# Performance work log

Measured on AMD Instinct MI355X. Metric: run time of the kernel, lower is better.

The kernel has to match this reference:

```python
import jax, jax.numpy as jnp
import numpy as np

N, E, G = 200000, 400000, 4096
EMB, FEAT, L = 300, 256, 5
NUM_ATOM, NUM_CHI, NUM_BOND, NUM_DIR = 119, 3, 5, 3


def setup_inputs() -> dict:
    key = jax.random.key(0)
    ks = jax.random.split(key, 24)
    s = 0.1
    return {
        "x": jax.random.randint(ks[0], (N, 2), 0, 3),
        "edge_index": jax.random.randint(ks[1], (2, E), 0, N),
        "edge_attr": jax.random.randint(ks[2], (E, 2), 0, 3),
        "batch": jnp.sort(jax.random.randint(ks[3], (N,), 0, G)),
        # node-type embeddings
        "x_emb1": jax.random.normal(ks[4], (NUM_ATOM, EMB)) * s,
        "x_emb2": jax.random.normal(ks[5], (NUM_CHI, EMB)) * s,
        # per-layer GCN params (stacked over L layers)
        "W": jax.random.normal(ks[6], (L, EMB, EMB)) * s,
        "b": jnp.zeros((L, EMB)),
        "e1": jax.random.normal(ks[7], (L, NUM_BOND, 1)) * s,
        "e2": jax.random.normal(ks[8], (L, NUM_DIR, 1)) * s,
        # batchnorm params
        "gamma": jnp.ones((L, EMB)),
        "beta": jnp.zeros((L, EMB)),
        # heads
        "feat_W": jax.random.normal(ks[9], (EMB, FEAT)) * s,
        "feat_b": jnp.zeros((FEAT,)),
        "out_W1": jax.random.normal(ks[10], (FEAT, FEAT)) * s,
        "out_b1": jnp.zeros((FEAT,)),
        "out_W2": jax.random.normal(ks[11], (FEAT, FEAT // 2)) * s,
        "out_b2": jnp.zeros((FEAT // 2,)),
    }


def reference(x, edge_index, edge_attr, batch, x_emb1, x_emb2, W, b, e1, e2,
              gamma, beta, feat_W, feat_b, out_W1, out_b1, out_W2, out_b2):
    n = x.shape[0]
    loop = jnp.arange(n, dtype=edge_index.dtype)
    # add self loops: edge type 4, direction 0
    src = jnp.concatenate([edge_index[0], loop])
    dst = jnp.concatenate([edge_index[1], loop])
    ea0 = jnp.concatenate([edge_attr[:, 0], jnp.full((n,), 4, edge_attr.dtype)])
    ea1 = jnp.concatenate([edge_attr[:, 1], jnp.zeros((n,), edge_attr.dtype)])

    h = x_emb1[x[:, 0]] + x_emb2[x[:, 1]]  # [N, EMB]
    for l in range(L):
        edge_emb = e1[l][ea0] + e2[l][ea1]           # [E+N, 1]
        hw = h @ W[l]                                 # [N, EMB]
        msg = hw[src] + edge_emb                      # gather + edge bias
        h = jax.ops.segment_sum(msg, dst, num_segments=n) + b[l]
        # batchnorm (training stats, biased var)
        mean = jnp.mean(h, axis=0)
        var = jnp.var(h, axis=0)
        h = (h - mean) * jax.lax.rsqrt(var + 1e-5) * gamma[l] + beta[l]
        if l < L - 1:
            h = jax.nn.relu(h)

    # global mean pool over graphs
    cnt = jax.ops.segment_sum(jnp.ones((n,), h.dtype), batch, num_segments=G)
    hg = jax.ops.segment_sum(h, batch, num_segments=G) / jnp.maximum(cnt, 1.0)[:, None]

    hf = hg @ feat_W + feat_b                         # [G, FEAT]
    out = jax.nn.relu(hf @ out_W1 + out_b1) @ out_W2 + out_b2  # [G, FEAT//2]
    return (hf, out)
```

## Files before the change

kernel.cpp:

```cpp
#include <hip/hip_runtime.h>

#define NN   200000
#define NE   400000
#define NG   4096
#define EMB  300
#define SD   304
#define SLOTS 38
#define NROW 200064
#define FEAT 256
#define LAYERS 5
#define NREP 16

typedef __attribute__((ext_vector_type(8))) short short8;
typedef __attribute__((ext_vector_type(4))) float f32x4;

__device__ __forceinline__ float bf2f(unsigned short u){
  union { unsigned int i; float f; } v; v.i = ((unsigned int)u) << 16; return v.f;
}
__device__ __forceinline__ unsigned short f2bf(float f){
  union { float f; unsigned int i; } v; v.f = f;
  return (unsigned short)((v.i + 0x7fffu + ((v.i >> 16) & 1u)) >> 16);
}

__global__ void k_wt(const float* __restrict__ W, unsigned short* __restrict__ Wt){
  int idx = blockIdx.x * 256 + threadIdx.x;
  if (idx >= LAYERS * 320 * SD) return;
  int l = idx / (320 * SD);
  int rem = idx - l * 320 * SD;
  int j = rem / SD, k = rem - (rem / SD) * SD;
  unsigned short v = 0;
  if (j < EMB && k < EMB) v = f2bf(W[l * EMB * EMB + k * EMB + j]);
  Wt[idx] = v;
}

__global__ __launch_bounds__(256) void k_embed(const int* __restrict__ x,
    const float* __restrict__ emb1, const float* __restrict__ emb2,
    unsigned short* __restrict__ H){
  __shared__ float e1s[900], e2s[900];
  int tid = threadIdx.x;
  for (int k = tid; k < 900; k += 256){ e1s[k] = emb1[k]; e2s[k] = emb2[k]; }
  __syncthreads();
  int t = blockIdx.x * 256 + tid;
  int i = t / SLOTS, c = t - (t / SLOTS) * SLOTS;
  if (i >= NN) return;
  int x0 = x[2 * i], x1 = x[2 * i + 1];
  int cb = c * 8;
  unsigned short o[8];
#pragma unroll
  for (int e = 0; e < 8; ++e){
    int col = cb + e; float v = 0.f;
    if (col < EMB) v = e1s[x0 * EMB + col] + e2s[x1 * EMB + col];
    o[e] = f2bf(v);
  }
  *reinterpret_cast<uint4*>(H + (size_t)i * SD + cb) = *reinterpret_cast<uint4*>(o);
}

__global__ void k_deg(const int* __restrict__ ei, int* __restrict__ deg){
  int e = blockIdx.x * 256 + threadIdx.x;
  if (e < NE) atomicAdd(&deg[ei[NE + e]], 1);
}
__global__ void k_scan1(const int* __restrict__ deg, int* __restrict__ incl, int* __restrict__ bsum){
  __shared__ int sm[256];
  int t = threadIdx.x; int i = blockIdx.x * 256 + t;
  int v = (i < NN) ? deg[i] : 0; sm[t] = v;
  for (int o = 1; o < 256; o <<= 1){
    __syncthreads(); int xx = (t >= o) ? sm[t - o] : 0;
    __syncthreads(); sm[t] += xx;
  }
  __syncthreads();
  if (i < NN) incl[i] = sm[t];
  if (t == 255) bsum[blockIdx.x] = sm[255];
}
__global__ void k_scan2(const int* __restrict__ bsum, int* __restrict__ bincl){
  __shared__ int sm[1024];
  int t = threadIdx.x;
  int v = (t < 782) ? bsum[t] : 0; sm[t] = v;
  for (int o = 1; o < 1024; o <<= 1){
    __syncthreads(); int xx = (t >= o) ? sm[t - o] : 0;
    __syncthreads(); sm[t] += xx;
  }
  __syncthreads();
  bincl[t] = sm[t];
}
__global__ void k_scan3(const int* __restrict__ incl, const int* __restrict__ deg,
    const int* __restrict__ bincl, int* __restrict__ rowPtr){
  int i = blockIdx.x * 256 + threadIdx.x;
  if (i < NN) rowPtr[i] = incl[i] - deg[i] + (blockIdx.x ? bincl[blockIdx.x - 1] : 0);
}
__global__ void k_fill(const int* __restrict__ ei, const int* __restrict__ ea,
    const int* __restrict__ rowPtr, int* __restrict__ cursor, int* __restrict__ csr){
  int e = blockIdx.x * 256 + threadIdx.x;
  if (e >= NE) return;
  int dst = ei[NE + e], src = ei[e];
  int code = ea[2 * e] * 3 + ea[2 * e + 1];
  int pos = atomicAdd(&cursor[dst], 1);
  csr[rowPtr[dst] + pos] = src | (code << 20);
}

__global__ __launch_bounds__(256, 2) void k_fused(
    const unsigned short* __restrict__ Hin, const unsigned short* __restrict__ Wt,
    const float2* __restrict__ st, const int* __restrict__ rowPtr,
    const int* __restrict__ deg, const int* __restrict__ csr,
    const float* __restrict__ e1l, const float* __restrict__ e2l,
    const float* __restrict__ bl, unsigned short* __restrict__ Hout,
    float* __restrict__ cs, int relu){
  __shared__ unsigned short bLds[64 * 320];
  __shared__ float2 stl[SD];
  __shared__ float eetab[9];
  __shared__ float eeself_s;
  __shared__ float cvl[64];
  int tid = threadIdx.x, lane = tid & 63, wave = tid >> 6;
  for (int j = tid; j < SD; j += 256) stl[j] = st[j];
  if (tid < 9) eetab[tid] = e1l[tid / 3] + e2l[tid % 3];
  if (tid == 9) eeself_s = e1l[4] + e2l[0];
  __syncthreads();
  int r0 = blockIdx.x * 64;
  int rloc = wave * 16 + (lane & 15);
  int row = r0 + rloc;
  int kg = lane >> 4;

  float accv[10][8];
#pragma unroll
  for (int m = 0; m < 10; ++m)
#pragma unroll
    for (int e = 0; e < 8; ++e) accv[m][e] = 0.f;

  auto addRow = [&](int src){
    const unsigned short* p = Hin + (size_t)src * SD + kg * 8;
#pragma unroll
    for (int m = 0; m < 10; ++m){
      if (m < 9 || kg < 2){
        uint4 v = *reinterpret_cast<const uint4*>(p + m * 32);
        unsigned int w[4] = {v.x, v.y, v.z, v.w};
        int cb = m * 32 + kg * 8;
#pragma unroll
        for (int e = 0; e < 8; ++e){
          unsigned short u = (e & 1) ? (unsigned short)(w[e >> 1] >> 16)
                                     : (unsigned short)(w[e >> 1] & 0xffff);
          float2 sv = stl[cb + e];
          float xv = sv.x * bf2f(u) + sv.y;
          if (relu) xv = fmaxf(xv, 0.f);
          accv[m][e] += xv;
        }
      }
    }
  };

  float csum = eeself_s;
  addRow(row);
  {
    int st0 = rowPtr[row], cnt = deg[row];
    for (int e = 0; e < cnt; ++e){
      int p = csr[st0 + e];
      csum += eetab[p >> 20];
      addRow(p & 0xFFFFF);
    }
  }
  if (kg == 0) cvl[rloc] = csum;

  short8 afr[10];
#pragma unroll
  for (int m = 0; m < 10; ++m){
    unsigned short o[8];
#pragma unroll
    for (int e = 0; e < 8; ++e) o[e] = f2bf(accv[m][e]);
    afr[m] = *reinterpret_cast<short8*>(o);
  }

  f32x4 acc[20];
#pragma unroll
  for (int a = 0; a < 20; ++a) acc[a] = (f32x4){0.f, 0.f, 0.f, 0.f};
#pragma unroll
  for (int jt = 0; jt < 5; ++jt){
    __syncthreads();
#pragma unroll
    for (int it = 0; it < 10; ++it){
      int s = it * 256 + tid;
      int jl = s / 40, cc = s - (s / 40) * 40;
      int srcC = cc ^ (jl & 7);
      uint4 v = make_uint4(0u, 0u, 0u, 0u);
      if (srcC < SLOTS)
        v = *reinterpret_cast<const uint4*>(Wt + ((size_t)(jt * 64 + jl) * SD + srcC * 8));
      *reinterpret_cast<uint4*>(&bLds[jl * 320 + cc * 8]) = v;
    }
    __syncthreads();
#pragma unroll
    for (int kc = 0; kc < 10; ++kc){
#pragma unroll
      for (int fl = 0; fl < 4; ++fl){
        int jl = fl * 16 + (lane & 15);
        int cw = kc * 4 + (lane >> 4);
        int cs_ = cw ^ (jl & 7);
        short8 bfr = *reinterpret_cast<const short8*>(&bLds[jl * 320 + cs_ * 8]);
        acc[jt * 4 + fl] = __builtin_amdgcn_mfma_f32_16x16x32_bf16(afr[kc], bfr, acc[jt * 4 + fl], 0, 0, 0);
      }
    }
  }
  __syncthreads();
  unsigned short* oLds = bLds;
  {
    int rb = wave * 16 + (lane >> 4) * 4;
#pragma unroll
    for (int r = 0; r < 4; ++r){
      int lrow = rb + r;
      float cv = cvl[lrow];
#pragma unroll
      for (int a = 0; a < 20; ++a){
        int col = (a >> 2) * 64 + (a & 3) * 16 + (lane & 15);
        if (col < SD){
          float bv = (col < EMB) ? bl[col] : 0.f;
          oLds[lrow * SD + col] = f2bf(acc[a][r] + cv + bv);
        }
      }
    }
  }
  __syncthreads();
  {
    float* csr_ = cs + (size_t)(blockIdx.x & (NREP - 1)) * 2 * SD;
    for (int c = tid; c < EMB; c += 256){
      float s = 0.f, s2 = 0.f;
#pragma unroll 4
      for (int r = 0; r < 64; ++r){
        float v = bf2f(oLds[r * SD + c]);
        s += v; s2 += v * v;
      }
      atomicAdd(&csr_[c], s); atomicAdd(&csr_[SD + c], s2);
    }
  }
  for (int s = tid; s < 64 * SLOTS; s += 256){
    *reinterpret_cast<uint4*>(Hout + (size_t)r0 * SD + s * 8) =
        *reinterpret_cast<const uint4*>(&bLds[(s / SLOTS) * SD + (s - (s / SLOTS) * SLOTS) * 8]);
  }
}

__global__ void k_stfin(const float* __restrict__ cs, const float* __restrict__ gam,
    const float* __restrict__ bet, float2* __restrict__ st){
  int j = threadIdx.x;
  if (j < EMB){
    float sm = 0.f, sq = 0.f;
    for (int r = 0; r < NREP; ++r){
      sm += cs[(size_t)r * 2 * SD + j];
      sq += cs[(size_t)r * 2 * SD + SD + j];
    }
    float mean = sm * (1.f / NN);
    float var = sq * (1.f / NN) - mean * mean;
    float rr = rsqrtf(var + 1e-5f);
    float s = gam[j] * rr;
    st[j] = make_float2(s, bet[j] - mean * s);
  } else if (j < SD) st[j] = make_float2(0.f, 0.f);
}
__global__ void k_stinit(float2* __restrict__ st){
  int j = threadIdx.x; if (j < SD) st[j] = make_float2(1.f, 0.f);
}

__global__ void k_pool(const unsigned short* __restrict__ H, const float2* __restrict__ st,
    const int* __restrict__ batch, float* __restrict__ hg){
  int gph = blockIdx.x, j = threadIdx.x;
  if (j >= SD) return;
  int lo, hi;
  { int a = 0, bn = NN; while (a < bn){ int m = (a + bn) >> 1; if (batch[m] < gph) a = m + 1; else bn = m; } lo = a; }
  { int a = lo, bn = NN; while (a < bn){ int m = (a + bn) >> 1; if (batch[m] < gph + 1) a = m + 1; else bn = m; } hi = a; }
  float acc = 0.f;
  for (int i = lo; i < hi; ++i) acc += bf2f(H[(size_t)i * SD + j]);
  int cnt = hi - lo;
  float2 sv = st[j];
  hg[gph * SD + j] = (sv.x * acc + (float)cnt * sv.y) / (float)max(cnt, 1);
}
__global__ __launch_bounds__(256) void k_head1(const float* __restrict__ hg,
    const float* __restrict__ fW, const float* __restrict__ fb,
    float* __restrict__ out0){
  __shared__ float row[EMB];
  int g = blockIdx.x, t = threadIdx.x;
  for (int j = t; j < EMB; j += 256) row[j] = hg[g * SD + j];
  __syncthreads();
  float acc = fb[t];
  for (int j = 0; j < EMB; ++j) acc += row[j] * fW[j * FEAT + t];
  out0[g * FEAT + t] = acc;
}
__global__ __launch_bounds__(256) void k_head2(const float* __restrict__ hf,
    const float* __restrict__ W1, const float* __restrict__ b1,
    const float* __restrict__ W2, const float* __restrict__ b2,
    float* __restrict__ out1){
  __shared__ float row[FEAT];
  __shared__ float t1[FEAT];
  int g = blockIdx.x, t = threadIdx.x;
  row[t] = hf[g * FEAT + t];
  __syncthreads();
  float acc = b1[t];
  for (int k = 0; k < FEAT; ++k) acc += row[k] * W1[k * FEAT + t];
  t1[t] = fmaxf(acc, 0.f);
  __syncthreads();
  if (t < 128){
    float a2 = b2[t];
    for (int k = 0; k < FEAT; ++k) a2 += t1[k] * W2[k * 128 + t];
    out1[g * 128 + t] = a2;
  }
}

extern "C" void kernel_launch(void* const* d_in, const int* in_sizes, int n_in,
                              void* d_out, int out_size, void* d_ws, size_t ws_size,
                              hipStream_t stream){
  const int* x   = (const int*)d_in[0];
  const int* ei  = (const int*)d_in[1];
  const int* ea  = (const int*)d_in[2];
  const int* bat = (const int*)d_in[3];
  const float* emb1 = (const float*)d_in[4];
  const float* emb2 = (const float*)d_in[5];
  const float* W    = (const float*)d_in[6];
  const float* bb   = (const float*)d_in[7];
  const float* e1   = (const float*)d_in[8];
  const float* e2   = (const float*)d_in[9];
  const float* gam  = (const float*)d_in[10];
  const float* bet  = (const float*)d_in[11];
  const float* fW   = (const float*)d_in[12];
  const float* fb   = (const float*)d_in[13];
  const float* oW1  = (const float*)d_in[14];
  const float* ob1  = (const float*)d_in[15];
  const float* oW2  = (const float*)d_in[16];
  const float* ob2  = (const float*)d_in[17];
  float* out = (float*)d_out;

  unsigned char* ws = (unsigned char*)d_ws;
  size_t off = 0;
  auto carve = [&](size_t bytes) -> void* {
    off = (off + 255) & ~(size_t)255;
    void* p = ws + off; off += bytes; return p;
  };
  const size_t SZ_H = (size_t)NROW * SD * 2;
  unsigned short* bufA = (unsigned short*)carve(SZ_H);
  unsigned short* bufB = (unsigned short*)carve(SZ_H);
  unsigned short* Wt = (unsigned short*)carve((size_t)LAYERS * 320 * SD * 2);
  int* deg     = (int*)carve((size_t)NN * 4);
  int* rowPtr  = (int*)carve((size_t)NN * 4);
  int* csr     = (int*)carve((size_t)NE * 4);
  int* bsum    = (int*)carve(1024 * 4);
  int* bincl   = (int*)carve(1024 * 4);
  float* colst = (float*)carve((size_t)NREP * 2 * SD * 4);
  float2* st   = (float2*)carve(SD * 8);
  size_t needed = off;
  if (ws_size < needed) return;

  int* incl    = (int*)bufB;
  int* cursor  = (int*)((unsigned char*)bufB + (size_t)NN * 4);
  float* hg    = (float*)bufA;

  hipMemsetAsync(deg, 0, (size_t)NN * 4, stream);
  hipMemsetAsync(cursor, 0, (size_t)NN * 4, stream);

  k_wt<<<(LAYERS * 320 * SD + 255) / 256, 256, 0, stream>>>(W, Wt);
  k_embed<<<(NN * SLOTS + 255) / 256, 256, 0, stream>>>(x, emb1, emb2, bufA);
  k_stinit<<<1, SD, 0, stream>>>(st);
  k_deg<<<(NE + 255) / 256, 256, 0, stream>>>(ei, deg);
  k_scan1<<<782, 256, 0, stream>>>(deg, incl, bsum);
  k_scan2<<<1, 1024, 0, stream>>>(bsum, bincl);
  k_scan3<<<782, 256, 0, stream>>>(incl, deg, bincl, rowPtr);
  k_fill<<<(NE + 255) / 256, 256, 0, stream>>>(ei, ea, rowPtr, cursor, csr);

  const unsigned short* hin = bufA;
  unsigned short* hout = bufB;
  for (int l = 0; l < LAYERS; ++l){
    hipMemsetAsync(colst, 0, (size_t)NREP * 2 * SD * 4, stream);
    k_fused<<<NN / 64, 256, 0, stream>>>(hin, Wt + (size_t)l * 320 * SD, st,
        rowPtr, deg, csr, e1 + l * 5, e2 + l * 3, bb + l * EMB,
        hout, colst, (l >= 1) ? 1 : 0);
    k_stfin<<<1, SD, 0, stream>>>(colst, gam + l * EMB, bet + l * EMB, st);
    const unsigned short* t = hin; hin = hout; hout = (unsigned short*)t;
  }

  k_pool<<<NG, 320, 0, stream>>>(hin, st, bat, hg);
  k_head1<<<NG, 256, 0, stream>>>(hg, fW, fb, out);
  k_head2<<<NG, 256, 0, stream>>>(out, oW1, ob1, oW2, ob2, out + (size_t)NG * FEAT);
}
```

Baseline: 2.757 ms.

## Software-pipeline neighbor row gathers in fused GCN kernel and raise occupancy hint

The neighbor aggregation loop becomes a double-buffered software pipeline. Each row is split into two halves, and the loads for the next source row are issued while the current halves are accumulated. The next CSR entry is also prefetched one iteration ahead. Launch bounds rise from 2 to 3 blocks per SU, which adds pressure on the register budget alongside the 40 extra held uint4 registers and may cause spills.

```diff
diff --git a/kernel.cpp b/kernel.cpp
--- a/kernel.cpp
+++ b/kernel.cpp
@@ -97,7 +97,7 @@
   csr[rowPtr[dst] + pos] = src | (code << 20);
 }
 
-__global__ __launch_bounds__(256, 2) void k_fused(
+__global__ __launch_bounds__(256, 3) void k_fused(
     const unsigned short* __restrict__ Hin, const unsigned short* __restrict__ Wt,
     const float2* __restrict__ st, const int* __restrict__ rowPtr,
     const int* __restrict__ deg, const int* __restrict__ csr,
@@ -125,14 +125,42 @@
 #pragma unroll
     for (int e = 0; e < 8; ++e) accv[m][e] = 0.f;
 
-  auto addRow = [&](int src){
+  uint4 h0[5], h1[5];
+  auto loadH0 = [&](int src){
     const unsigned short* p = Hin + (size_t)src * SD + kg * 8;
 #pragma unroll
-    for (int m = 0; m < 10; ++m){
-      if (m < 9 || kg < 2){
-        uint4 v = *reinterpret_cast<const uint4*>(p + m * 32);
-        unsigned int w[4] = {v.x, v.y, v.z, v.w};
-        int cb = m * 32 + kg * 8;
+    for (int m = 0; m < 5; ++m)
+      h0[m] = *reinterpret_cast<const uint4*>(p + m * 32);
+  };
+  auto loadH1 = [&](int src){
+    const unsigned short* p = Hin + (size_t)src * SD + kg * 8 + 160;
+#pragma unroll
+    for (int m = 0; m < 5; ++m)
+      if (m < 4 || kg < 2)
+        h1[m] = *reinterpret_cast<const uint4*>(p + m * 32);
+  };
+  auto accH0 = [&](){
+#pragma unroll
+    for (int m = 0; m < 5; ++m){
+      unsigned int w[4] = {h0[m].x, h0[m].y, h0[m].z, h0[m].w};
+      int cb = m * 32 + kg * 8;
+#pragma unroll
+      for (int e = 0; e < 8; ++e){
+        unsigned short u = (e & 1) ? (unsigned short)(w[e >> 1] >> 16)
+                                   : (unsigned short)(w[e >> 1] & 0xffff);
+        float2 sv = stl[cb + e];
+        float xv = sv.x * bf2f(u) + sv.y;
+        if (relu) xv = fmaxf(xv, 0.f);
+        accv[m][e] += xv;
+      }
+    }
+  };
+  auto accH1 = [&](){
+#pragma unroll
+    for (int m = 0; m < 5; ++m){
+      if (m < 4 || kg < 2){
+        unsigned int w[4] = {h1[m].x, h1[m].y, h1[m].z, h1[m].w};
+        int cb = (m + 5) * 32 + kg * 8;
 #pragma unroll
         for (int e = 0; e < 8; ++e){
           unsigned short u = (e & 1) ? (unsigned short)(w[e >> 1] >> 16)
@@ -140,22 +168,29 @@
           float2 sv = stl[cb + e];
           float xv = sv.x * bf2f(u) + sv.y;
           if (relu) xv = fmaxf(xv, 0.f);
-          accv[m][e] += xv;
+          accv[m + 5][e] += xv;
         }
       }
     }
   };
 
   float csum = eeself_s;
-  addRow(row);
-  {
-    int st0 = rowPtr[row], cnt = deg[row];
+  int st0 = rowPtr[row], cnt = deg[row];
+  loadH0(row); loadH1(row);
+  if (cnt > 0){
+    int pc = csr[st0];
     for (int e = 0; e < cnt; ++e){
-      int p = csr[st0 + e];
-      csum += eetab[p >> 20];
-      addRow(p & 0xFFFFF);
-    }
-  }
+      int pn = (e + 1 < cnt) ? csr[st0 + e + 1] : 0;
+      csum += eetab[pc >> 20];
+      int src = pc & 0xFFFFF;
+      accH0();
+      loadH0(src);
+      accH1();
+      loadH1(src);
+      pc = pn;
+    }
+  }
+  accH0(); accH1();
   if (kg == 0) cvl[rloc] = csum;
 
   short8 afr[10];
```

New measurement: 7.138 ms. 159% more time.

## Restructure neighbor gather with 8-lane row groups, double-buffered loads, and LDS staging

Applied to the files above, without the earlier changes.

The aggregation phase now assigns 8 threads per destination row and processes the 64 rows in two passes of 32. Each neighbor's row loads are double-buffered, so the next neighbor's global loads are issued before the current one is consumed. Aggregated bf16 rows are written to a swizzled LDS tile and then read back as MFMA A fragments, which cuts the per-thread accumulator registers. This is meant to hide gather latency and to raise occupancy to 3 blocks per CU, at the cost of an extra LDS round trip and extra synchronization.

```diff
diff --git a/kernel.cpp b/kernel.cpp
--- a/kernel.cpp
+++ b/kernel.cpp
@@ -97,14 +97,14 @@
   csr[rowPtr[dst] + pos] = src | (code << 20);
 }
 
-__global__ __launch_bounds__(256, 2) void k_fused(
+__global__ __launch_bounds__(256, 3) void k_fused(
     const unsigned short* __restrict__ Hin, const unsigned short* __restrict__ Wt,
     const float2* __restrict__ st, const int* __restrict__ rowPtr,
     const int* __restrict__ deg, const int* __restrict__ csr,
     const float* __restrict__ e1l, const float* __restrict__ e2l,
     const float* __restrict__ bl, unsigned short* __restrict__ Hout,
     float* __restrict__ cs, int relu){
-  __shared__ unsigned short bLds[64 * 320];
+  __shared__ unsigned short tLds[64 * 320];
   __shared__ float2 stl[SD];
   __shared__ float eetab[9];
   __shared__ float eeself_s;
@@ -115,56 +115,101 @@
   if (tid == 9) eeself_s = e1l[4] + e2l[0];
   __syncthreads();
   int r0 = blockIdx.x * 64;
-  int rloc = wave * 16 + (lane & 15);
-  int row = r0 + rloc;
+  int g = tid & 7;
+
+#pragma unroll 1
+  for (int pass = 0; pass < 2; ++pass){
+    int rloc = pass * 32 + (tid >> 3);
+    int row = r0 + rloc;
+    float accv[5][8];
+#pragma unroll
+    for (int q = 0; q < 5; ++q)
+#pragma unroll
+      for (int e = 0; e < 8; ++e) accv[q][e] = 0.f;
+
+    uint4 sA[5], sB[5];
+    auto issueA = [&](int src){
+      const unsigned short* p = Hin + (size_t)src * SD;
+#pragma unroll
+      for (int q = 0; q < 5; ++q){
+        int ch = q * 8 + g;
+        if (ch < SLOTS) sA[q] = *reinterpret_cast<const uint4*>(p + ch * 8);
+      }
+    };
+    auto issueB = [&](int src){
+      const unsigned short* p = Hin + (size_t)src * SD;
+#pragma unroll
+      for (int q = 0; q < 5; ++q){
+        int ch = q * 8 + g;
+        if (ch < SLOTS) sB[q] = *reinterpret_cast<const uint4*>(p + ch * 8);
+      }
+    };
+    auto consume = [&](const uint4 (&s)[5]){
+#pragma unroll
+      for (int q = 0; q < 5; ++q){
+        int ch = q * 8 + g;
+        if (ch < SLOTS){
+          unsigned int w[4] = {s[q].x, s[q].y, s[q].z, s[q].w};
+          int cb = ch * 8;
+#pragma unroll
+          for (int e = 0; e < 8; ++e){
+            unsigned short u = (e & 1) ? (unsigned short)(w[e >> 1] >> 16)
+                                       : (unsigned short)(w[e >> 1] & 0xffff);
+            float2 sv = stl[cb + e];
+            float xv = sv.x * bf2f(u) + sv.y;
+            if (relu) xv = fmaxf(xv, 0.f);
+            accv[q][e] += xv;
+          }
+        }
+      }
+    };
+
+    float csum = eeself_s;
+    int st0 = rowPtr[row], cnt = deg[row];
+    issueA(row);
+    int e = 0;
+    for (; e + 1 < cnt; e += 2){
+      int p0 = csr[st0 + e];
+      csum += eetab[p0 >> 20];
+      issueB(p0 & 0xFFFFF);
+      consume(sA);
+      int p1 = csr[st0 + e + 1];
+      csum += eetab[p1 >> 20];
+      issueA(p1 & 0xFFFFF);
+      consume(sB);
+    }
+    if (e < cnt){
+      int p0 = csr[st0 + e];
+      csum += eetab[p0 >> 20];
+      issueB(p0 & 0xFFFFF);
+      consume(sA);
+      consume(sB);
+    } else {
+      consume(sA);
+    }
+    if (g == 0) cvl[rloc] = csum;
+
+#pragma unroll
+    for (int q = 0; q < 5; ++q){
+      int ch = q * 8 + g;
+      int p = ch ^ (rloc & 7);
+      unsigned short o[8];
+#pragma unroll
+      for (int e2_ = 0; e2_ < 8; ++e2_)
+        o[e2_] = (ch < SLOTS) ? f2bf(accv[q][e2_]) : (unsigned short)0;
+      *reinterpret_cast<uint4*>(&tLds[rloc * 320 + p * 8]) = *reinterpret_cast<uint4*>(o);
+    }
+  }
+  __syncthreads();
+
   int kg = lane >> 4;
-
-  float accv[10][8];
-#pragma unroll
-  for (int m = 0; m < 10; ++m)
-#pragma unroll
-    for (int e = 0; e < 8; ++e) accv[m][e] = 0.f;
-
-  auto addRow = [&](int src){
-    const unsigned short* p = Hin + (size_t)src * SD + kg * 8;
-#pragma unroll
-    for (int m = 0; m < 10; ++m){
-      if (m < 9 || kg < 2){
-        uint4 v = *reinterpret_cast<const uint4*>(p + m * 32);
-        unsigned int w[4] = {v.x, v.y, v.z, v.w};
-        int cb = m * 32 + kg * 8;
-#pragma unroll
-        for (int e = 0; e < 8; ++e){
-          unsigned short u = (e & 1) ? (unsigned short)(w[e >> 1] >> 16)
-                                     : (unsigned short)(w[e >> 1] & 0xffff);
-          float2 sv = stl[cb + e];
-          float xv = sv.x * bf2f(u) + sv.y;
-          if (relu) xv = fmaxf(xv, 0.f);
-          accv[m][e] += xv;
-        }
-      }
-    }
-  };
-
-  float csum = eeself_s;
-  addRow(row);
-  {
-    int st0 = rowPtr[row], cnt = deg[row];
-    for (int e = 0; e < cnt; ++e){
-      int p = csr[st0 + e];
-      csum += eetab[p >> 20];
-      addRow(p & 0xFFFFF);
-    }
-  }
-  if (kg == 0) cvl[rloc] = csum;
-
+  int rr = wave * 16 + (lane & 15);
   short8 afr[10];
 #pragma unroll
   for (int m = 0; m < 10; ++m){
-    unsigned short o[8];
-#pragma unroll
-    for (int e = 0; e < 8; ++e) o[e] = f2bf(accv[m][e]);
-    afr[m] = *reinterpret_cast<short8*>(o);
+    int c = m * 4 + kg;
+    int p = c ^ (rr & 7);
+    afr[m] = *reinterpret_cast<const short8*>(&tLds[rr * 320 + p * 8]);
   }
 
   f32x4 acc[20];
@@ -181,7 +226,7 @@
       uint4 v = make_uint4(0u, 0u, 0u, 0u);
       if (srcC < SLOTS)
         v = *reinterpret_cast<const uint4*>(Wt + ((size_t)(jt * 64 + jl) * SD + srcC * 8));
-      *reinterpret_cast<uint4*>(&bLds[jl * 320 + cc * 8]) = v;
+      *reinterpret_cast<uint4*>(&tLds[jl * 320 + cc * 8]) = v;
     }
     __syncthreads();
 #pragma unroll
@@ -191,13 +236,13 @@
         int jl = fl * 16 + (lane & 15);
         int cw = kc * 4 + (lane >> 4);
         int cs_ = cw ^ (jl & 7);
-        short8 bfr = *reinterpret_cast<const short8*>(&bLds[jl * 320 + cs_ * 8]);
+        short8 bfr = *reinterpret_cast<const short8*>(&tLds[jl * 320 + cs_ * 8]);
         acc[jt * 4 + fl] = __builtin_amdgcn_mfma_f32_16x16x32_bf16(afr[kc], bfr, acc[jt * 4 + fl], 0, 0, 0);
       }
     }
   }
   __syncthreads();
-  unsigned short* oLds = bLds;
+  unsigned short* oLds = tLds;
   {
     int rb = wave * 16 + (lane >> 4) * 4;
 #pragma unroll
@@ -229,7 +274,7 @@
   }
   for (int s = tid; s < 64 * SLOTS; s += 256){
     *reinterpret_cast<uint4*>(Hout + (size_t)r0 * SD + s * 8) =
-        *reinterpret_cast<const uint4*>(&bLds[(s / SLOTS) * SD + (s - (s / SLOTS) * SLOTS) * 8]);
+        *reinterpret_cast<const uint4*>(&tLds[(s / SLOTS) * SD + (s - (s / SLOTS) * SLOTS) * 8]);
   }
 }
 
```

Result: faster. 2.416 ms (-12.4%).
